# Optimization experiments

Hardware: AMD Instinct MI355X
Metric: run time of the kernel (lower is better)

Reference implementation:

```python
import jax, jax.numpy as jnp
import numpy as np

N_RNA, N_ATAC = 4096, 8192
IN_C, HID, H = 256, 128, 2
DH = HID // H
TOPK, THR = 10, 0.8


def setup_inputs() -> dict:
    key = jax.random.key(0)
    ks = jax.random.split(key, 16)
    s = 0.02
    inp = {
        'x_rna': jax.random.normal(ks[0], (N_RNA, IN_C), jnp.float32),
        'x_atac': jax.random.normal(ks[1], (N_ATAC, IN_C), jnp.float32),
        'chrom_mask': (jax.random.uniform(ks[2], (N_RNA, N_ATAC)) > 0.5).astype(jnp.float32),
        'Wq': jax.random.normal(ks[3], (IN_C, HID)) * s, 'bq': jnp.zeros((HID,)),
        'Wk': jax.random.normal(ks[4], (IN_C, HID)) * s, 'bk': jnp.zeros((HID,)),
        'Wvr': jax.random.normal(ks[5], (IN_C, HID)) * s, 'bvr': jnp.zeros((HID,)),
        'Wva': jax.random.normal(ks[6], (IN_C, HID)) * s, 'bva': jnp.zeros((HID,)),
        'Wor': jax.random.normal(ks[7], (HID, HID)) * s, 'bor': jnp.zeros((HID,)),
        'Woa': jax.random.normal(ks[8], (HID, HID)) * s, 'boa': jnp.zeros((HID,)),
        'Wsr': jax.random.normal(ks[9], (IN_C, HID)) * s, 'bsr': jnp.zeros((HID,)),
        'Wsa': jax.random.normal(ks[10], (IN_C, HID)) * s, 'bsa': jnp.zeros((HID,)),
        'Wdr': jax.random.normal(ks[11], (2 * HID, HID)) * s, 'bdr': jnp.zeros((HID,)),
        'Wda': jax.random.normal(ks[12], (2 * HID, HID)) * s, 'bda': jnp.zeros((HID,)),
    }
    return inp


def reference(x_rna, x_atac, chrom_mask, Wq, bq, Wk, bk, Wvr, bvr, Wva, bva,
              Wor, bor, Woa, boa, Wsr, bsr, Wsa, bsa, Wdr, bdr, Wda, bda):
    # projections -> [N, H, DH]
    q = (x_rna @ Wq + bq).reshape(N_RNA, H, DH)
    k = (x_atac @ Wk + bk).reshape(N_ATAC, H, DH)
    v_a = (x_atac @ Wva + bva).reshape(N_ATAC, H, DH)
    v_r = (x_rna @ Wvr + bvr).reshape(N_RNA, H, DH)

    # raw attention [H, N_rna, N_atac], biological mask, sigmoid
    att = jnp.einsum('rhd,ahd->hra', q, k) * chrom_mask[None]
    att = jax.nn.sigmoid(att)
    thr_mask = (att > THR).astype(att.dtype)

    # top-k sparsify + softmax over selected values, scatter back
    topv, topi = jax.lax.top_k(att, TOPK)          # [H, N_rna, K]
    topv = jax.nn.softmax(topv, axis=-1)
    i_h = jnp.arange(H)[:, None, None]
    i_r = jnp.arange(N_RNA)[None, :, None]
    sparse = jnp.zeros_like(att).at[i_h, i_r, topi].set(topv)
    att = sparse * thr_mask

    # aggregations (second bmm and its transpose)
    rna_agg = jnp.einsum('hra,ahd->rhd', att, v_a).reshape(N_RNA, HID)
    atac_agg = jnp.einsum('hra,rhd->ahd', att, v_r).reshape(N_ATAC, HID)

    # out proj (num_heads > 1), self attention concat, dim reduction
    rna_agg = rna_agg @ Wor + bor
    atac_agg = atac_agg @ Woa + boa
    rna_agg = jnp.concatenate([rna_agg, x_rna @ Wsr + bsr], axis=1)
    atac_agg = jnp.concatenate([atac_agg, x_atac @ Wsa + bsa], axis=1)
    return (rna_agg @ Wdr + bdr, atac_agg @ Wda + bda)
```

## Files before the change

### kernel.cpp

```cpp
#include <hip/hip_runtime.h>
#include <math.h>

#define N_RNA 4096
#define N_ATAC 8192
#define IN_C 256
#define HID 128
#define NH 2
#define TOPK 10
#define CAP 32
#define NCHUNK 8
#define TAU_EPS 0.12f
#define NEG_INF -3.402823466e38f

typedef __attribute__((ext_vector_type(8))) short bf16x8;
typedef __attribute__((ext_vector_type(4))) float f32x4;

static __device__ __forceinline__ f32x4 mfma16(bf16x8 a, bf16x8 b, f32x4 c) {
    return __builtin_amdgcn_mfma_f32_16x16x32_bf16(a, b, c, 0, 0, 0);
}

static __device__ __forceinline__ unsigned short f2bf(float f) {
    unsigned int u = __float_as_uint(f);
    unsigned int r = (u + 0x7fffu + ((u >> 16) & 1u)) >> 16;
    return (unsigned short)r;
}
static __device__ __forceinline__ float bf2f(unsigned short h) {
    return __uint_as_float(((unsigned int)h) << 16);
}

__global__ __launch_bounds__(256) void wprep(
    const float* __restrict__ Wq, const float* __restrict__ Wk,
    const float* __restrict__ Wvr, const float* __restrict__ Wva,
    const float* __restrict__ Wor, const float* __restrict__ bor,
    const float* __restrict__ Woa, const float* __restrict__ boa,
    const float* __restrict__ Wsr, const float* __restrict__ bsr,
    const float* __restrict__ Wsa, const float* __restrict__ bsa,
    const float* __restrict__ Wdr, const float* __restrict__ bdr,
    const float* __restrict__ Wda, const float* __restrict__ bda,
    unsigned short* __restrict__ wt, unsigned short* __restrict__ wrf,
    unsigned short* __restrict__ waf,
    float* __restrict__ brf, float* __restrict__ baf) {
    int bx = blockIdx.x, tid = threadIdx.x;
    if (bx < 32) {
        int cfg = bx >> 3, k0 = (bx & 7) * 32;
        const float* W = (cfg == 0) ? Wq : (cfg == 1) ? Wvr : (cfg == 2) ? Wk : Wva;
        __shared__ float ts[32][132];
#pragma unroll
        for (int rep = 0; rep < 4; ++rep) {
            int id = rep * 256 + tid; int kk = id >> 5, cq = id & 31;
            float4 v = *(const float4*)&W[(size_t)(k0 + kk) * HID + cq * 4];
            ts[kk][cq * 4 + 0] = v.x; ts[kk][cq * 4 + 1] = v.y;
            ts[kk][cq * 4 + 2] = v.z; ts[kk][cq * 4 + 3] = v.w;
        }
        __syncthreads();
        int col = tid >> 1, seg = tid & 1;
        unsigned short hb[16], lb[16];
#pragma unroll
        for (int u = 0; u < 16; ++u) {
            float f = ts[seg * 16 + u][col];
            unsigned short h = f2bf(f);
            hb[u] = h; lb[u] = f2bf(f - bf2f(h));
        }
        unsigned short* hp = wt + cfg * 65536;
        unsigned short* lp = hp + 32768;
        size_t o = (size_t)col * 256 + k0 + seg * 16;
#pragma unroll
        for (int u4 = 0; u4 < 4; ++u4) {
            ushort4 th, tl;
            th.x = hb[u4 * 4]; th.y = hb[u4 * 4 + 1]; th.z = hb[u4 * 4 + 2]; th.w = hb[u4 * 4 + 3];
            tl.x = lb[u4 * 4]; tl.y = lb[u4 * 4 + 1]; tl.z = lb[u4 * 4 + 2]; tl.w = lb[u4 * 4 + 3];
            *(ushort4*)&hp[o + u4 * 4] = th;
            *(ushort4*)&lp[o + u4 * 4] = tl;
        }
        return;
    }
    int f = (bx - 32) * 256 + tid;
    if (f < 16384) {
        int i = f >> 7, j = f & 127; float s = 0.f;
        for (int t = 0; t < 128; ++t) s += Wor[i * 128 + t] * Wdr[t * 128 + j];
        unsigned short h = f2bf(s);
        wrf[(size_t)j * 128 + i] = h;
        wrf[16384 + (size_t)j * 128 + i] = f2bf(s - bf2f(h));
    } else if (f < 49152) {
        int e = f - 16384; int i = e >> 7, j = e & 127; float s = 0.f;
        for (int t = 0; t < 128; ++t) s += Wsr[i * 128 + t] * Wdr[(128 + t) * 128 + j];
        unsigned short h = f2bf(s);
        wrf[32768 + (size_t)j * 256 + i] = h;
        wrf[65536 + (size_t)j * 256 + i] = f2bf(s - bf2f(h));
    } else if (f < 65536) {
        int e = f - 49152; int i = e >> 7, j = e & 127; float s = 0.f;
        for (int t = 0; t < 128; ++t) s += Woa[i * 128 + t] * Wda[t * 128 + j];
        unsigned short h = f2bf(s);
        waf[(size_t)j * 128 + i] = h;
        waf[16384 + (size_t)j * 128 + i] = f2bf(s - bf2f(h));
    } else if (f < 98304) {
        int e = f - 65536; int i = e >> 7, j = e & 127; float s = 0.f;
        for (int t = 0; t < 128; ++t) s += Wsa[i * 128 + t] * Wda[(128 + t) * 128 + j];
        unsigned short h = f2bf(s);
        waf[32768 + (size_t)j * 256 + i] = h;
        waf[65536 + (size_t)j * 256 + i] = f2bf(s - bf2f(h));
    } else if (f < 98432) {
        int j = f - 98304; float s = bdr[j];
        for (int t = 0; t < 128; ++t) s += bor[t] * Wdr[t * 128 + j] + bsr[t] * Wdr[(128 + t) * 128 + j];
        brf[j] = s;
    } else if (f < 98560) {
        int j = f - 98432; float s = bda[j];
        for (int t = 0; t < 128; ++t) s += boa[t] * Wda[t * 128 + j] + bsa[t] * Wda[(128 + t) * 128 + j];
        baf[j] = s;
    }
}

__global__ __launch_bounds__(256) void prep_all(
    const float* __restrict__ mask, unsigned int* __restrict__ bits2,
    float* __restrict__ atac_agg,
    const float* __restrict__ x_rna, const float* __restrict__ x_atac,
    const unsigned short* __restrict__ wt,
    const float* __restrict__ bq, const float* __restrict__ bk,
    const float* __restrict__ bvr, const float* __restrict__ bva,
    unsigned short* __restrict__ qhi, unsigned short* __restrict__ khf_hi,
    float* __restrict__ q_f32, float* __restrict__ k_f32,
    float* __restrict__ v_r, float* __restrict__ v_a) {
    __shared__ __align__(16) unsigned short ah_s[32 * 40];
    __shared__ __align__(16) unsigned short al_s[32 * 40];
    int bx = blockIdx.x, tid = threadIdx.x;

    if (bx >= 768 && bx < 1280) {
        int e = bx - 768;
        int rt = e >> 3, ac = e & 7;
        int a0 = ac * 1024 + tid * 4;
        int r0 = rt * 64;
        unsigned int w0[4] = {0, 0, 0, 0}, w1[4] = {0, 0, 0, 0};
#pragma unroll 8
        for (int rr = 0; rr < 32; ++rr) {
            float4 m0 = *(const float4*)&mask[(size_t)(r0 + rr) * N_ATAC + a0];
            float4 m1 = *(const float4*)&mask[(size_t)(r0 + 32 + rr) * N_ATAC + a0];
            w0[0] |= ((m0.x > 0.5f) ? 1u : 0u) << rr;
            w0[1] |= ((m0.y > 0.5f) ? 1u : 0u) << rr;
            w0[2] |= ((m0.z > 0.5f) ? 1u : 0u) << rr;
            w0[3] |= ((m0.w > 0.5f) ? 1u : 0u) << rr;
            w1[0] |= ((m1.x > 0.5f) ? 1u : 0u) << rr;
            w1[1] |= ((m1.y > 0.5f) ? 1u : 0u) << rr;
            w1[2] |= ((m1.z > 0.5f) ? 1u : 0u) << rr;
            w1[3] |= ((m1.w > 0.5f) ? 1u : 0u) << rr;
        }
        uint4 oA = make_uint4(w0[0], w1[0], w0[1], w1[1]);
        uint4 oB = make_uint4(w0[2], w1[2], w0[3], w1[3]);
        *(uint4*)&bits2[((size_t)rt * N_ATAC + a0) * 2] = oA;
        *(uint4*)&bits2[((size_t)rt * N_ATAC + a0) * 2 + 4] = oB;
        return;
    }
    if (bx >= 1280) {
        size_t i = ((size_t)(bx - 1280) * 256 + tid) * 16;
        float4 z = make_float4(0.f, 0.f, 0.f, 0.f);
        *(float4*)&atac_agg[i] = z;
        *(float4*)&atac_agg[i + 4] = z;
        *(float4*)&atac_agg[i + 8] = z;
        *(float4*)&atac_agg[i + 12] = z;
        return;
    }

    int cfg, rblk;
    if (bx < 128)      { cfg = 0; rblk = bx; }
    else if (bx < 256) { cfg = 1; rblk = bx - 128; }
    else if (bx < 512) { cfg = 2; rblk = bx - 256; }
    else               { cfg = 3; rblk = bx - 512; }
    const float* X = (cfg <= 1) ? x_rna : x_atac;
    const float* Bv = (cfg == 0) ? bq : (cfg == 1) ? bvr : (cfg == 2) ? bk : bva;
    const unsigned short* wth = wt + cfg * 65536;
    const unsigned short* wtl = wth + 32768;
    int r0 = rblk * 32;
    int w = tid >> 6, lane = tid & 63, n = lane & 15, quad = lane >> 4;

    const f32x4 zf = {0.f, 0.f, 0.f, 0.f};
    f32x4 acc[2][2];
#pragma unroll
    for (int mt = 0; mt < 2; ++mt)
#pragma unroll
        for (int nt = 0; nt < 2; ++nt) acc[mt][nt] = zf;

    for (int k0 = 0; k0 < IN_C; k0 += 32) {
        __syncthreads();
        {
            int rr = tid >> 3, kq = tid & 7;
            float4 v = *(const float4*)&X[(size_t)(r0 + rr) * IN_C + k0 + kq * 4];
            ushort4 h, l;
            h.x = f2bf(v.x); h.y = f2bf(v.y); h.z = f2bf(v.z); h.w = f2bf(v.w);
            l.x = f2bf(v.x - bf2f(h.x)); l.y = f2bf(v.y - bf2f(h.y));
            l.z = f2bf(v.z - bf2f(h.z)); l.w = f2bf(v.w - bf2f(h.w));
            *(ushort4*)&ah_s[rr * 40 + kq * 4] = h;
            *(ushort4*)&al_s[rr * 40 + kq * 4] = l;
        }
        __syncthreads();
        bf16x8 Afh[2], Afl[2];
#pragma unroll
        for (int mt = 0; mt < 2; ++mt) {
            Afh[mt] = *(const bf16x8*)&ah_s[(mt * 16 + n) * 40 + quad * 8];
            Afl[mt] = *(const bf16x8*)&al_s[(mt * 16 + n) * 40 + quad * 8];
        }
#pragma unroll
        for (int nt = 0; nt < 2; ++nt) {
            int c = w * 32 + nt * 16 + n;
            size_t o = (size_t)c * 256 + k0 + quad * 8;
            bf16x8 Bh = *(const bf16x8*)&wth[o];
            bf16x8 Bl = *(const bf16x8*)&wtl[o];
#pragma unroll
            for (int mt = 0; mt < 2; ++mt) {
                acc[mt][nt] = mfma16(Afh[mt], Bh, acc[mt][nt]);
                acc[mt][nt] = mfma16(Afh[mt], Bl, acc[mt][nt]);
                acc[mt][nt] = mfma16(Afl[mt], Bh, acc[mt][nt]);
            }
        }
    }
    float bvx[2];
    bvx[0] = Bv[w * 32 + n]; bvx[1] = Bv[w * 32 + 16 + n];
    if (cfg == 1 || cfg == 3) {
        float* C = (cfg == 1) ? v_r : v_a;
#pragma unroll
        for (int mt = 0; mt < 2; ++mt)
#pragma unroll
            for (int nt = 0; nt < 2; ++nt)
#pragma unroll
                for (int i = 0; i < 4; ++i) {
                    int r = r0 + mt * 16 + quad * 4 + i;
                    int c = w * 32 + nt * 16 + n;
                    C[(size_t)r * HID + c] = acc[mt][nt][i] + bvx[nt];
                }
    } else if (cfg == 0) {
#pragma unroll
        for (int mt = 0; mt < 2; ++mt)
#pragma unroll
            for (int nt = 0; nt < 2; ++nt)
#pragma unroll
                for (int i = 0; i < 4; ++i) {
                    int r = r0 + mt * 16 + quad * 4 + i;
                    int c = w * 32 + nt * 16 + n;
                    float o = acc[mt][nt][i] + bvx[nt];
                    int head = c >> 6, ch = c & 63;
                    size_t off = ((size_t)head * N_RNA + r) * 64 + ch;
                    qhi[off] = f2bf(o);
                    q_f32[(size_t)r * HID + c] = o;
                }
    } else {
#pragma unroll
        for (int mt = 0; mt < 2; ++mt)
#pragma unroll
            for (int nt = 0; nt < 2; ++nt)
#pragma unroll
                for (int i = 0; i < 4; ++i) {
                    int r = r0 + mt * 16 + quad * 4 + i;
                    int c = w * 32 + nt * 16 + n;
                    float o = acc[mt][nt][i] + bvx[nt];
                    int head = c >> 6, ch = c & 63;
                    size_t off = ((size_t)(head * 512 + (r >> 4)) * 8 + (ch >> 3)) * 128
                               + (size_t)(r & 15) * 8 + (ch & 7);
                    khf_hi[off] = f2bf(o);
                    k_f32[(size_t)r * HID + c] = o;
                }
    }
}

__global__ __launch_bounds__(256, 4) void attn2(
    const unsigned short* __restrict__ qhi, const unsigned short* __restrict__ khf_hi,
    const unsigned int* __restrict__ bits2, const float* __restrict__ q_f32,
    const float* __restrict__ k_f32,
    int* __restrict__ scnt, float* __restrict__ sval, int* __restrict__ sidx) {
    int hq = blockIdx.x; int h = hq >> 3, chunk = hq & 7;
    int rt = blockIdx.y; int r0 = rt * 32;
    int tid = threadIdx.x;
    int w = tid >> 6, lane = tid & 63;
    int n = lane & 15, quad = lane >> 4;
    int q4 = quad * 4;
    int at0 = chunk * 64 + w * 16;
    int hbase = h * 512;
    int rt64 = rt >> 1, word = rt & 1;

    __shared__ __align__(16) float smem[32 * 65];
    __shared__ __align__(16) float q_s[32][68];
    __shared__ float taus[32];
    __shared__ int   lcnt[32];

    const bf16x8* kh8 = (const bf16x8*)khf_hi;

    bf16x8 Ah[2][2];
#pragma unroll
    for (int mt = 0; mt < 2; ++mt)
#pragma unroll
        for (int c = 0; c < 2; ++c) {
            size_t off = ((size_t)h * N_RNA + r0 + mt * 16 + n) * 64 + c * 32 + quad * 8;
            Ah[mt][c] = *(const bf16x8*)(qhi + off);
        }

    float mx[2][4];
#pragma unroll
    for (int mt = 0; mt < 2; ++mt)
#pragma unroll
        for (int i = 0; i < 4; ++i) mx[mt][i] = 0.f;

#pragma unroll 2
    for (int t = 0; t < 16; ++t) {
        int at = at0 + t;
        size_t bidx = ((size_t)hbase + at) * 128 + lane;
        bf16x8 Bh0 = kh8[bidx];
        bf16x8 Bh1 = kh8[bidx + 64];
        unsigned int bw = bits2[((size_t)rt64 * N_ATAC + at * 16 + n) * 2 + word];

        f32x4 S[2];
#pragma unroll
        for (int mt = 0; mt < 2; ++mt) {
            f32x4 s = {0.f, 0.f, 0.f, 0.f};
            s = mfma16(Ah[mt][0], Bh0, s);
            s = mfma16(Ah[mt][1], Bh1, s);
            S[mt] = s;
        }
#pragma unroll
        for (int mt = 0; mt < 2; ++mt) {
            unsigned int sh = bw >> ((mt << 4) + q4);
#pragma unroll
            for (int i = 0; i < 4; ++i) {
                float v = ((sh >> i) & 1) ? S[mt][i] : 0.f;
                mx[mt][i] = fmaxf(mx[mt][i], v);
            }
        }
    }

    {
        int b = w * 16 + n;
#pragma unroll
        for (int mt = 0; mt < 2; ++mt)
#pragma unroll
            for (int i = 0; i < 4; ++i) smem[(mt * 16 + q4 + i) * 65 + b] = mx[mt][i];
    }
    __syncthreads();
    {
        int row = tid >> 3, sub = tid & 7;
        float v[8];
#pragma unroll
        for (int j = 0; j < 8; ++j) v[j] = smem[row * 65 + sub * 8 + j];
        float t10 = 0.f;
#pragma unroll
        for (int s = 0; s < 10; ++s) {
            float bv = v[0]; int bj = 0;
#pragma unroll
            for (int j = 1; j < 8; ++j) if (v[j] > bv) { bv = v[j]; bj = j; }
            int meta = (sub << 3) | bj;
#pragma unroll
            for (int off = 1; off < 8; off <<= 1) {
                float ov = __shfl_xor(bv, off);
                int om = __shfl_xor(meta, off);
                if (ov > bv || (ov == bv && om < meta)) { bv = ov; meta = om; }
            }
            if ((meta >> 3) == sub) v[meta & 7] = -1.f;
            t10 = bv;
        }
        if (sub == 0) taus[row] = t10 - TAU_EPS;
        if (tid < 32) lcnt[tid] = 0;
    }
    {
        for (int i4 = tid; i4 < 512; i4 += 256) {
            int row = i4 >> 4, dq = (i4 & 15) * 4;
            *(float4*)&q_s[row][dq] =
                *(const float4*)&q_f32[(size_t)(r0 + row) * HID + h * 64 + dq];
        }
    }
    __syncthreads();

    float tau[2][4];
#pragma unroll
    for (int mt = 0; mt < 2; ++mt)
#pragma unroll
        for (int i = 0; i < 4; ++i) tau[mt][i] = taus[mt * 16 + q4 + i];

    int* lidx = (int*)smem;

#pragma unroll 2
    for (int t = 0; t < 16; ++t) {
        int at = at0 + t;
        size_t bidx = ((size_t)hbase + at) * 128 + lane;
        bf16x8 Bh0 = kh8[bidx];
        bf16x8 Bh1 = kh8[bidx + 64];
        unsigned int bw = bits2[((size_t)rt64 * N_ATAC + at * 16 + n) * 2 + word];

        f32x4 S[2];
#pragma unroll
        for (int mt = 0; mt < 2; ++mt) {
            f32x4 s = {0.f, 0.f, 0.f, 0.f};
            s = mfma16(Ah[mt][0], Bh0, s);
            s = mfma16(Ah[mt][1], Bh1, s);
            S[mt] = s;
        }
        int a16 = at * 16 + n;
#pragma unroll
        for (int mt = 0; mt < 2; ++mt) {
            unsigned int sh = bw >> ((mt << 4) + q4);
#pragma unroll
            for (int i = 0; i < 4; ++i) {
                if (((sh >> i) & 1) && S[mt][i] >= tau[mt][i]) {
                    int row = mt * 16 + q4 + i;
                    int pos = atomicAdd(&lcnt[row], 1);
                    if (pos < CAP) lidx[row * CAP + pos] = a16;
                }
            }
        }
    }
    __syncthreads();

    if (tid < 32) {
        int c = lcnt[tid]; if (c > CAP) c = CAP;
        scnt[((size_t)h * N_RNA + r0 + tid) * NCHUNK + chunk] = c;
    }
    {
        int gi = tid >> 3, sub = tid & 7;
        int c = lcnt[gi]; if (c > CAP) c = CAP;
        size_t slot = ((size_t)h * N_RNA + r0 + gi) * NCHUNK + chunk;
        float4 qa = *(const float4*)&q_s[gi][sub * 8];
        float4 qb = *(const float4*)&q_s[gi][sub * 8 + 4];
        for (int j = 0; j < c; ++j) {
            int a = lidx[gi * CAP + j];
            const float* kr = &k_f32[(size_t)a * HID + h * 64 + sub * 8];
            float4 ka = *(const float4*)kr;
            float4 kb = *(const float4*)(kr + 4);
            float s = qa.x * ka.x + qa.y * ka.y + qa.z * ka.z + qa.w * ka.w
                    + qb.x * kb.x + qb.y * kb.y + qb.z * kb.z + qb.w * kb.w;
            s += __shfl_xor(s, 1); s += __shfl_xor(s, 2); s += __shfl_xor(s, 4);
            if (sub == 0) sval[slot * CAP + j] = s;
            if (sub == 1) sidx[slot * CAP + j] = a;
        }
    }
}

__global__ __launch_bounds__(256) void fin_agg(
    const int* __restrict__ scnt, const float* __restrict__ sval, const int* __restrict__ sidx,
    const float* __restrict__ v_a, const float* __restrict__ v_r,
    float* __restrict__ rna_agg, float* __restrict__ atac_agg) {
    int wid = threadIdx.x >> 6, lane = threadIdx.x & 63;
    int p = blockIdx.x * 4 + wid;
    int h = p >> 12, r = p & 4095;
    size_t sbase = (size_t)p * NCHUNK;

    float val[4]; int aidx[4];
#pragma unroll
    for (int j = 0; j < 4; ++j) {
        int e = j * 64 + lane;
        int chunk = e >> 5, pos = e & 31;
        int c = scnt[sbase + chunk];
        size_t sl = (sbase + chunk) * CAP + pos;
        bool ok = pos < c;
        val[j] = ok ? sval[sl] : NEG_INF;
        aidx[j] = ok ? sidx[sl] : 0;
    }

    float sv[10]; int si[10];
#pragma unroll
    for (int s = 0; s < 10; ++s) {
        float bv = val[0]; int bj = 0;
#pragma unroll
        for (int j = 1; j < 4; ++j) if (val[j] > bv) { bv = val[j]; bj = j; }
        int bmeta = (bj << 6) | lane;
#pragma unroll
        for (int off = 32; off >= 1; off >>= 1) {
            float ov = __shfl_xor(bv, off);
            int om = __shfl_xor(bmeta, off);
            if (ov > bv || (ov == bv && om < bmeta)) { bv = ov; bmeta = om; }
        }
        int wj = bmeta >> 6, wl = bmeta & 63;
        if (lane == wl) {
#pragma unroll
            for (int j = 0; j < 4; ++j) if (j == wj) val[j] = NEG_INF;
        }
        int av = aidx[0];
#pragma unroll
        for (int j = 1; j < 4; ++j) if (wj == j) av = aidx[j];
        sv[s] = bv;
        si[s] = __shfl(av, wl);
    }

    float wgt[10]; float sum = 0.f; float sg[10];
#pragma unroll
    for (int s = 0; s < 10; ++s) {
        sg[s] = 1.0f / (1.0f + expf(-sv[s]));
        float es = expf(sg[s]);
        wgt[s] = es;
        sum += es;
    }
    float inv = 1.0f / sum;
#pragma unroll
    for (int s = 0; s < 10; ++s) {
        wgt[s] *= inv;
        if (!(sg[s] > 0.8f)) wgt[s] = 0.f;
    }

    float acc = 0.f;
#pragma unroll
    for (int s = 0; s < 10; ++s) {
        float vv = v_a[(size_t)si[s] * HID + h * 64 + lane];
        acc += wgt[s] * vv;
    }
    rna_agg[(size_t)r * HID + h * 64 + lane] = acc;

    float vr = v_r[(size_t)r * HID + h * 64 + lane];
#pragma unroll
    for (int s = 0; s < 10; ++s) {
        if (wgt[s] != 0.f) {
            atomicAdd(&atac_agg[(size_t)si[s] * HID + h * 64 + lane], wgt[s] * vr);
        }
    }
}

__global__ __launch_bounds__(256) void out_gemm(
    const float* __restrict__ rna_agg, const float* __restrict__ x_rna,
    const unsigned short* __restrict__ wrt, const float* __restrict__ brf,
    const float* __restrict__ atac_agg, const float* __restrict__ x_atac,
    const unsigned short* __restrict__ wat, const float* __restrict__ baf,
    float* __restrict__ out_r, float* __restrict__ out_a) {
    __shared__ __align__(16) unsigned short ah_s[32 * 40];
    __shared__ __align__(16) unsigned short al_s[32 * 40];
    int bx = blockIdx.x, tid = threadIdx.x;
    const float *A, *X, *bias; const unsigned short* wb; float* C; int r0;
    if (bx < 128) { A = rna_agg; X = x_rna; wb = wrt; bias = brf; C = out_r; r0 = bx * 32; }
    else { A = atac_agg; X = x_atac; wb = wat; bias = baf; C = out_a; r0 = (bx - 128) * 32; }
    int w = tid >> 6, lane = tid & 63, n = lane & 15, quad = lane >> 4;

    const f32x4 zf = {0.f, 0.f, 0.f, 0.f};
    f32x4 acc[2][2];
#pragma unroll
    for (int mt = 0; mt < 2; ++mt)
#pragma unroll
        for (int nt = 0; nt < 2; ++nt) acc[mt][nt] = zf;

    for (int k0 = 0; k0 < 384; k0 += 32) {
        __syncthreads();
        {
            int rr = tid >> 3, kq = tid & 7;
            float4 v;
            if (k0 < 128) v = *(const float4*)&A[(size_t)(r0 + rr) * HID + k0 + kq * 4];
            else          v = *(const float4*)&X[(size_t)(r0 + rr) * IN_C + (k0 - 128) + kq * 4];
            ushort4 h, l;
            h.x = f2bf(v.x); h.y = f2bf(v.y); h.z = f2bf(v.z); h.w = f2bf(v.w);
            l.x = f2bf(v.x - bf2f(h.x)); l.y = f2bf(v.y - bf2f(h.y));
            l.z = f2bf(v.z - bf2f(h.z)); l.w = f2bf(v.w - bf2f(h.w));
            *(ushort4*)&ah_s[rr * 40 + kq * 4] = h;
            *(ushort4*)&al_s[rr * 40 + kq * 4] = l;
        }
        __syncthreads();
        bf16x8 Afh[2], Afl[2];
#pragma unroll
        for (int mt = 0; mt < 2; ++mt) {
            Afh[mt] = *(const bf16x8*)&ah_s[(mt * 16 + n) * 40 + quad * 8];
            Afl[mt] = *(const bf16x8*)&al_s[(mt * 16 + n) * 40 + quad * 8];
        }
#pragma unroll
        for (int nt = 0; nt < 2; ++nt) {
            int c = w * 32 + nt * 16 + n;
            size_t o;
            const unsigned short *ph, *pl;
            if (k0 < 128) { o = (size_t)c * 128 + k0 + quad * 8;         ph = wb;         pl = wb + 16384; }
            else          { o = (size_t)c * 256 + (k0 - 128) + quad * 8; ph = wb + 32768; pl = wb + 65536; }
            bf16x8 Bh = *(const bf16x8*)&ph[o];
            bf16x8 Bl = *(const bf16x8*)&pl[o];
#pragma unroll
            for (int mt = 0; mt < 2; ++mt) {
                acc[mt][nt] = mfma16(Afh[mt], Bh, acc[mt][nt]);
                acc[mt][nt] = mfma16(Afh[mt], Bl, acc[mt][nt]);
                acc[mt][nt] = mfma16(Afl[mt], Bh, acc[mt][nt]);
            }
        }
    }
    float bvx[2];
    bvx[0] = bias[w * 32 + n]; bvx[1] = bias[w * 32 + 16 + n];
#pragma unroll
    for (int mt = 0; mt < 2; ++mt)
#pragma unroll
        for (int nt = 0; nt < 2; ++nt)
#pragma unroll
            for (int i = 0; i < 4; ++i) {
                int r = r0 + mt * 16 + quad * 4 + i;
                int c = w * 32 + nt * 16 + n;
                C[(size_t)r * HID + c] = acc[mt][nt][i] + bvx[nt];
            }
}

extern "C" void kernel_launch(void* const* d_in, const int* in_sizes, int n_in,
                              void* d_out, int out_size, void* d_ws, size_t ws_size,
                              hipStream_t stream) {
    const float* x_rna = (const float*)d_in[0];
    const float* x_atac = (const float*)d_in[1];
    const float* mask = (const float*)d_in[2];
    const float* Wq = (const float*)d_in[3];  const float* bq = (const float*)d_in[4];
    const float* Wk = (const float*)d_in[5];  const float* bk = (const float*)d_in[6];
    const float* Wvr = (const float*)d_in[7]; const float* bvr = (const float*)d_in[8];
    const float* Wva = (const float*)d_in[9]; const float* bva = (const float*)d_in[10];
    const float* Wor = (const float*)d_in[11]; const float* bor = (const float*)d_in[12];
    const float* Woa = (const float*)d_in[13]; const float* boa = (const float*)d_in[14];
    const float* Wsr = (const float*)d_in[15]; const float* bsr = (const float*)d_in[16];
    const float* Wsa = (const float*)d_in[17]; const float* bsa = (const float*)d_in[18];
    const float* Wdr = (const float*)d_in[19]; const float* bdr = (const float*)d_in[20];
    const float* Wda = (const float*)d_in[21]; const float* bda = (const float*)d_in[22];

    float* out_r = (float*)d_out;
    float* out_a = out_r + N_RNA * HID;

    float* ws = (float*)d_ws;
    unsigned short* qhi = (unsigned short*)ws;
    unsigned short* khf_hi = qhi + 524288;
    float* q_f32 = ws + 786432;
    float* k_f32 = q_f32 + 524288;
    unsigned int* bits2 = (unsigned int*)(k_f32 + 1048576);
    float* v_r = (float*)(bits2 + 1048576);
    float* v_a = v_r + 524288;
    unsigned short* wrf = (unsigned short*)(v_a + 1048576);
    float* brf = (float*)(wrf + 98304);
    unsigned short* waf = (unsigned short*)(brf + 128);
    float* baf = (float*)(waf + 98304);
    int* scnt = (int*)(baf + 128);
    float* sval = (float*)(scnt + 65536);
    int* sidx = (int*)(sval + 2097152);
    float* rna_agg = (float*)(sidx + 2097152);
    float* atac_agg = rna_agg + 524288;
    unsigned short* wt = (unsigned short*)(atac_agg + 1048576);

    hipLaunchKernelGGL(wprep, dim3(417), dim3(256), 0, stream,
                       Wq, Wk, Wvr, Wva,
                       Wor, bor, Woa, boa, Wsr, bsr, Wsa, bsa, Wdr, bdr, Wda, bda,
                       wt, wrf, waf, brf, baf);
    hipLaunchKernelGGL(prep_all, dim3(1536), dim3(256), 0, stream,
                       mask, bits2, atac_agg, x_rna, x_atac, wt,
                       bq, bk, bvr, bva,
                       qhi, khf_hi, q_f32, k_f32, v_r, v_a);
    hipLaunchKernelGGL(attn2, dim3(16, 128), dim3(256), 0, stream,
                       qhi, khf_hi, bits2, q_f32, k_f32, scnt, sval, sidx);
    hipLaunchKernelGGL(fin_agg, dim3(2048), dim3(256), 0, stream,
                       scnt, sval, sidx, v_a, v_r, rna_agg, atac_agg);
    hipLaunchKernelGGL(out_gemm, dim3(384), dim3(256), 0, stream,
                       rna_agg, x_rna, wrf, brf,
                       atac_agg, x_atac, waf, baf, out_r, out_a);
}
```

Baseline: 386.0 us.

## Cache masked attention scores in registers; move fused-weight prep into prep_all

The attn2 kernel now keeps all 16 tiles of masked scores in a register array from the first pass and reuses them in the threshold-selection pass, instead of reloading K tiles and recomputing the MFMA products. To fit that register array, launch bounds drop from 4 to 2 blocks per SM, which lowers occupancy. Separately, the fused output-weight products (Wor·Wdr etc.) move out of wprep into extra blocks of prep_all. That shortens the serial wprep launch and lets the work overlap with mask packing and projections.

```diff
diff --git a/kernel.cpp b/kernel.cpp
--- a/kernel.cpp
+++ b/kernel.cpp
@@ -11,6 +11,7 @@
 #define NCHUNK 8
 #define TAU_EPS 0.12f
 #define NEG_INF -3.402823466e38f
+#define NEGL -1.0e30f
 
 typedef __attribute__((ext_vector_type(8))) short bf16x8;
 typedef __attribute__((ext_vector_type(4))) float f32x4;
@@ -31,82 +32,37 @@
 __global__ __launch_bounds__(256) void wprep(
     const float* __restrict__ Wq, const float* __restrict__ Wk,
     const float* __restrict__ Wvr, const float* __restrict__ Wva,
-    const float* __restrict__ Wor, const float* __restrict__ bor,
-    const float* __restrict__ Woa, const float* __restrict__ boa,
-    const float* __restrict__ Wsr, const float* __restrict__ bsr,
-    const float* __restrict__ Wsa, const float* __restrict__ bsa,
-    const float* __restrict__ Wdr, const float* __restrict__ bdr,
-    const float* __restrict__ Wda, const float* __restrict__ bda,
-    unsigned short* __restrict__ wt, unsigned short* __restrict__ wrf,
-    unsigned short* __restrict__ waf,
-    float* __restrict__ brf, float* __restrict__ baf) {
+    unsigned short* __restrict__ wt) {
     int bx = blockIdx.x, tid = threadIdx.x;
-    if (bx < 32) {
-        int cfg = bx >> 3, k0 = (bx & 7) * 32;
-        const float* W = (cfg == 0) ? Wq : (cfg == 1) ? Wvr : (cfg == 2) ? Wk : Wva;
-        __shared__ float ts[32][132];
-#pragma unroll
-        for (int rep = 0; rep < 4; ++rep) {
-            int id = rep * 256 + tid; int kk = id >> 5, cq = id & 31;
-            float4 v = *(const float4*)&W[(size_t)(k0 + kk) * HID + cq * 4];
-            ts[kk][cq * 4 + 0] = v.x; ts[kk][cq * 4 + 1] = v.y;
-            ts[kk][cq * 4 + 2] = v.z; ts[kk][cq * 4 + 3] = v.w;
-        }
-        __syncthreads();
-        int col = tid >> 1, seg = tid & 1;
-        unsigned short hb[16], lb[16];
-#pragma unroll
-        for (int u = 0; u < 16; ++u) {
-            float f = ts[seg * 16 + u][col];
-            unsigned short h = f2bf(f);
-            hb[u] = h; lb[u] = f2bf(f - bf2f(h));
-        }
-        unsigned short* hp = wt + cfg * 65536;
-        unsigned short* lp = hp + 32768;
-        size_t o = (size_t)col * 256 + k0 + seg * 16;
-#pragma unroll
-        for (int u4 = 0; u4 < 4; ++u4) {
-            ushort4 th, tl;
-            th.x = hb[u4 * 4]; th.y = hb[u4 * 4 + 1]; th.z = hb[u4 * 4 + 2]; th.w = hb[u4 * 4 + 3];
-            tl.x = lb[u4 * 4]; tl.y = lb[u4 * 4 + 1]; tl.z = lb[u4 * 4 + 2]; tl.w = lb[u4 * 4 + 3];
-            *(ushort4*)&hp[o + u4 * 4] = th;
-            *(ushort4*)&lp[o + u4 * 4] = tl;
-        }
-        return;
-    }
-    int f = (bx - 32) * 256 + tid;
-    if (f < 16384) {
-        int i = f >> 7, j = f & 127; float s = 0.f;
-        for (int t = 0; t < 128; ++t) s += Wor[i * 128 + t] * Wdr[t * 128 + j];
-        unsigned short h = f2bf(s);
-        wrf[(size_t)j * 128 + i] = h;
-        wrf[16384 + (size_t)j * 128 + i] = f2bf(s - bf2f(h));
-    } else if (f < 49152) {
-        int e = f - 16384; int i = e >> 7, j = e & 127; float s = 0.f;
-        for (int t = 0; t < 128; ++t) s += Wsr[i * 128 + t] * Wdr[(128 + t) * 128 + j];
-        unsigned short h = f2bf(s);
-        wrf[32768 + (size_t)j * 256 + i] = h;
-        wrf[65536 + (size_t)j * 256 + i] = f2bf(s - bf2f(h));
-    } else if (f < 65536) {
-        int e = f - 49152; int i = e >> 7, j = e & 127; float s = 0.f;
-        for (int t = 0; t < 128; ++t) s += Woa[i * 128 + t] * Wda[t * 128 + j];
-        unsigned short h = f2bf(s);
-        waf[(size_t)j * 128 + i] = h;
-        waf[16384 + (size_t)j * 128 + i] = f2bf(s - bf2f(h));
-    } else if (f < 98304) {
-        int e = f - 65536; int i = e >> 7, j = e & 127; float s = 0.f;
-        for (int t = 0; t < 128; ++t) s += Wsa[i * 128 + t] * Wda[(128 + t) * 128 + j];
-        unsigned short h = f2bf(s);
-        waf[32768 + (size_t)j * 256 + i] = h;
-        waf[65536 + (size_t)j * 256 + i] = f2bf(s - bf2f(h));
-    } else if (f < 98432) {
-        int j = f - 98304; float s = bdr[j];
-        for (int t = 0; t < 128; ++t) s += bor[t] * Wdr[t * 128 + j] + bsr[t] * Wdr[(128 + t) * 128 + j];
-        brf[j] = s;
-    } else if (f < 98560) {
-        int j = f - 98432; float s = bda[j];
-        for (int t = 0; t < 128; ++t) s += boa[t] * Wda[t * 128 + j] + bsa[t] * Wda[(128 + t) * 128 + j];
-        baf[j] = s;
+    int cfg = bx >> 3, k0 = (bx & 7) * 32;
+    const float* W = (cfg == 0) ? Wq : (cfg == 1) ? Wvr : (cfg == 2) ? Wk : Wva;
+    __shared__ float ts[32][132];
+#pragma unroll
+    for (int rep = 0; rep < 4; ++rep) {
+        int id = rep * 256 + tid; int kk = id >> 5, cq = id & 31;
+        float4 v = *(const float4*)&W[(size_t)(k0 + kk) * HID + cq * 4];
+        ts[kk][cq * 4 + 0] = v.x; ts[kk][cq * 4 + 1] = v.y;
+        ts[kk][cq * 4 + 2] = v.z; ts[kk][cq * 4 + 3] = v.w;
+    }
+    __syncthreads();
+    int col = tid >> 1, seg = tid & 1;
+    unsigned short hb[16], lb[16];
+#pragma unroll
+    for (int u = 0; u < 16; ++u) {
+        float f = ts[seg * 16 + u][col];
+        unsigned short h = f2bf(f);
+        hb[u] = h; lb[u] = f2bf(f - bf2f(h));
+    }
+    unsigned short* hp = wt + cfg * 65536;
+    unsigned short* lp = hp + 32768;
+    size_t o = (size_t)col * 256 + k0 + seg * 16;
+#pragma unroll
+    for (int u4 = 0; u4 < 4; ++u4) {
+        ushort4 th, tl;
+        th.x = hb[u4 * 4]; th.y = hb[u4 * 4 + 1]; th.z = hb[u4 * 4 + 2]; th.w = hb[u4 * 4 + 3];
+        tl.x = lb[u4 * 4]; tl.y = lb[u4 * 4 + 1]; tl.z = lb[u4 * 4 + 2]; tl.w = lb[u4 * 4 + 3];
+        *(ushort4*)&hp[o + u4 * 4] = th;
+        *(ushort4*)&lp[o + u4 * 4] = tl;
     }
 }
 
@@ -117,6 +73,14 @@
     const unsigned short* __restrict__ wt,
     const float* __restrict__ bq, const float* __restrict__ bk,
     const float* __restrict__ bvr, const float* __restrict__ bva,
+    const float* __restrict__ Wor, const float* __restrict__ bor,
+    const float* __restrict__ Woa, const float* __restrict__ boa,
+    const float* __restrict__ Wsr, const float* __restrict__ bsr,
+    const float* __restrict__ Wsa, const float* __restrict__ bsa,
+    const float* __restrict__ Wdr, const float* __restrict__ bdr,
+    const float* __restrict__ Wda, const float* __restrict__ bda,
+    unsigned short* __restrict__ wrf, unsigned short* __restrict__ waf,
+    float* __restrict__ brf, float* __restrict__ baf,
     unsigned short* __restrict__ qhi, unsigned short* __restrict__ khf_hi,
     float* __restrict__ q_f32, float* __restrict__ k_f32,
     float* __restrict__ v_r, float* __restrict__ v_a) {
@@ -149,13 +113,50 @@
         *(uint4*)&bits2[((size_t)rt * N_ATAC + a0) * 2 + 4] = oB;
         return;
     }
-    if (bx >= 1280) {
+    if (bx >= 1280 && bx < 1536) {
         size_t i = ((size_t)(bx - 1280) * 256 + tid) * 16;
         float4 z = make_float4(0.f, 0.f, 0.f, 0.f);
         *(float4*)&atac_agg[i] = z;
         *(float4*)&atac_agg[i + 4] = z;
         *(float4*)&atac_agg[i + 8] = z;
         *(float4*)&atac_agg[i + 12] = z;
+        return;
+    }
+    if (bx >= 1536) {
+        int f = (bx - 1536) * 256 + tid;
+        if (f < 16384) {
+            int i = f >> 7, j = f & 127; float s = 0.f;
+            for (int t = 0; t < 128; ++t) s += Wor[i * 128 + t] * Wdr[t * 128 + j];
+            unsigned short h = f2bf(s);
+            wrf[(size_t)j * 128 + i] = h;
+            wrf[16384 + (size_t)j * 128 + i] = f2bf(s - bf2f(h));
+        } else if (f < 49152) {
+            int e = f - 16384; int i = e >> 7, j = e & 127; float s = 0.f;
+            for (int t = 0; t < 128; ++t) s += Wsr[i * 128 + t] * Wdr[(128 + t) * 128 + j];
+            unsigned short h = f2bf(s);
+            wrf[32768 + (size_t)j * 256 + i] = h;
+            wrf[65536 + (size_t)j * 256 + i] = f2bf(s - bf2f(h));
+        } else if (f < 65536) {
+            int e = f - 49152; int i = e >> 7, j = e & 127; float s = 0.f;
+            for (int t = 0; t < 128; ++t) s += Woa[i * 128 + t] * Wda[t * 128 + j];
+            unsigned short h = f2bf(s);
+            waf[(size_t)j * 128 + i] = h;
+            waf[16384 + (size_t)j * 128 + i] = f2bf(s - bf2f(h));
+        } else if (f < 98304) {
+            int e = f - 65536; int i = e >> 7, j = e & 127; float s = 0.f;
+            for (int t = 0; t < 128; ++t) s += Wsa[i * 128 + t] * Wda[(128 + t) * 128 + j];
+            unsigned short h = f2bf(s);
+            waf[32768 + (size_t)j * 256 + i] = h;
+            waf[65536 + (size_t)j * 256 + i] = f2bf(s - bf2f(h));
+        } else if (f < 98432) {
+            int j = f - 98304; float s = bdr[j];
+            for (int t = 0; t < 128; ++t) s += bor[t] * Wdr[t * 128 + j] + bsr[t] * Wdr[(128 + t) * 128 + j];
+            brf[j] = s;
+        } else if (f < 98560) {
+            int j = f - 98432; float s = bda[j];
+            for (int t = 0; t < 128; ++t) s += boa[t] * Wda[t * 128 + j] + bsa[t] * Wda[(128 + t) * 128 + j];
+            baf[j] = s;
+        }
         return;
     }
 
@@ -259,7 +260,7 @@
     }
 }
 
-__global__ __launch_bounds__(256, 4) void attn2(
+__global__ __launch_bounds__(256, 2) void attn2(
     const unsigned short* __restrict__ qhi, const unsigned short* __restrict__ khf_hi,
     const unsigned int* __restrict__ bits2, const float* __restrict__ q_f32,
     const float* __restrict__ k_f32,
@@ -296,7 +297,9 @@
 #pragma unroll
         for (int i = 0; i < 4; ++i) mx[mt][i] = 0.f;
 
-#pragma unroll 2
+    float Sreg[16][8];
+
+#pragma unroll
     for (int t = 0; t < 16; ++t) {
         int at = at0 + t;
         size_t bidx = ((size_t)hbase + at) * 128 + lane;
@@ -317,8 +320,10 @@
             unsigned int sh = bw >> ((mt << 4) + q4);
 #pragma unroll
             for (int i = 0; i < 4; ++i) {
-                float v = ((sh >> i) & 1) ? S[mt][i] : 0.f;
-                mx[mt][i] = fmaxf(mx[mt][i], v);
+                bool on = (sh >> i) & 1;
+                float sv_ = S[mt][i];
+                mx[mt][i] = fmaxf(mx[mt][i], on ? sv_ : 0.f);
+                Sreg[t][mt * 4 + i] = on ? sv_ : NEGL;
             }
         }
     }
@@ -372,29 +377,14 @@
 
     int* lidx = (int*)smem;
 
-#pragma unroll 2
+#pragma unroll
     for (int t = 0; t < 16; ++t) {
-        int at = at0 + t;
-        size_t bidx = ((size_t)hbase + at) * 128 + lane;
-        bf16x8 Bh0 = kh8[bidx];
-        bf16x8 Bh1 = kh8[bidx + 64];
-        unsigned int bw = bits2[((size_t)rt64 * N_ATAC + at * 16 + n) * 2 + word];
-
-        f32x4 S[2];
+        int a16 = (at0 + t) * 16 + n;
 #pragma unroll
         for (int mt = 0; mt < 2; ++mt) {
-            f32x4 s = {0.f, 0.f, 0.f, 0.f};
-            s = mfma16(Ah[mt][0], Bh0, s);
-            s = mfma16(Ah[mt][1], Bh1, s);
-            S[mt] = s;
-        }
-        int a16 = at * 16 + n;
-#pragma unroll
-        for (int mt = 0; mt < 2; ++mt) {
-            unsigned int sh = bw >> ((mt << 4) + q4);
 #pragma unroll
             for (int i = 0; i < 4; ++i) {
-                if (((sh >> i) & 1) && S[mt][i] >= tau[mt][i]) {
+                if (Sreg[t][mt * 4 + i] >= tau[mt][i]) {
                     int row = mt * 16 + q4 + i;
                     int pos = atomicAdd(&lcnt[row], 1);
                     if (pos < CAP) lidx[row * CAP + pos] = a16;
@@ -618,13 +608,13 @@
     float* atac_agg = rna_agg + 524288;
     unsigned short* wt = (unsigned short*)(atac_agg + 1048576);
 
-    hipLaunchKernelGGL(wprep, dim3(417), dim3(256), 0, stream,
-                       Wq, Wk, Wvr, Wva,
-                       Wor, bor, Woa, boa, Wsr, bsr, Wsa, bsa, Wdr, bdr, Wda, bda,
-                       wt, wrf, waf, brf, baf);
-    hipLaunchKernelGGL(prep_all, dim3(1536), dim3(256), 0, stream,
+    hipLaunchKernelGGL(wprep, dim3(32), dim3(256), 0, stream,
+                       Wq, Wk, Wvr, Wva, wt);
+    hipLaunchKernelGGL(prep_all, dim3(1921), dim3(256), 0, stream,
                        mask, bits2, atac_agg, x_rna, x_atac, wt,
                        bq, bk, bvr, bva,
+                       Wor, bor, Woa, boa, Wsr, bsr, Wsa, bsa, Wdr, bdr, Wda, bda,
+                       wrf, waf, brf, baf,
                        qhi, khf_hi, q_f32, k_f32, v_r, v_a);
     hipLaunchKernelGGL(attn2, dim3(16, 128), dim3(256), 0, stream,
                        qhi, khf_hi, bits2, q_f32, k_f32, scnt, sval, sidx);
```

Result: slower. 438.2 us (+13.5%).
